# Kernel tuning notes

Hardware: AMD Instinct MI355X
Metric: run time of the kernel (lower is better)

Reference implementation:

```python
import jax, jax.numpy as jnp
import numpy as np

FUSION_RATIO = 0.1


def graph_conv(src, dst, x, W, b, n):
    # DGL GraphConv, norm='both': h = D_in^{-1/2} A D_out^{-1/2} (x W) + b
    ones = jnp.ones((src.shape[0],), x.dtype)
    deg_out = jnp.clip(jax.ops.segment_sum(ones, src, num_segments=n), 1.0)
    deg_in = jnp.clip(jax.ops.segment_sum(ones, dst, num_segments=n), 1.0)
    h = (x @ W) * (deg_out ** -0.5)[:, None]
    agg = jax.ops.segment_sum(h[src], dst, num_segments=n)  # [n, out]
    return agg * (deg_in ** -0.5)[:, None] + b


def norm_embed(e):
    # z-score (unbiased std, matching torch.std) then min-max
    e = (e - e.mean()) / jnp.std(e, ddof=1)
    return (e - e.min()) / (e.max() - e.min())


def setup_inputs() -> dict:
    key = jax.random.key(0)
    ks = jax.random.split(key, 24)
    n_apig, n_fcg = 50000, 100000
    e_apig, e_fcg = 800000, 1600000
    apig_dim, fcg_dim, hidden, united, ncls = 256, 128, 128, 64, 10
    s = 0.05
    inp = {
        'apig_feat': jax.random.normal(ks[0], (n_apig, apig_dim), jnp.float32),
        'fcg_feat': jax.random.normal(ks[1], (n_fcg, fcg_dim), jnp.float32),
        'W_a1': jax.random.normal(ks[2], (apig_dim, hidden), jnp.float32) * s,
        'b_a1': jnp.zeros((hidden,), jnp.float32),
        'W_a2': jax.random.normal(ks[3], (hidden, hidden), jnp.float32) * s,
        'b_a2': jnp.zeros((hidden,), jnp.float32),
        'W_f1': jax.random.normal(ks[4], (fcg_dim, hidden), jnp.float32) * s,
        'b_f1': jnp.zeros((hidden,), jnp.float32),
        'W_f2': jax.random.normal(ks[5], (hidden, hidden), jnp.float32) * s,
        'b_f2': jnp.zeros((hidden,), jnp.float32),
        'W1': jax.random.normal(ks[6], (hidden, united), jnp.float32) * s,
        'b1': jnp.zeros((united,), jnp.float32),
        'W2': jax.random.normal(ks[7], (united, hidden), jnp.float32) * s,
        'b2': jnp.zeros((hidden,), jnp.float32),
        'W_attn': jax.random.normal(ks[8], (hidden, 1), jnp.float32) * s,
        'b_attn': jnp.zeros((1,), jnp.float32),
        'W_cls': jax.random.normal(ks[9], (hidden, ncls), jnp.float32) * s,
        'b_cls': jnp.zeros((ncls,), jnp.float32),
        'apig_src': jax.random.randint(ks[10], (e_apig,), 0, n_apig, jnp.int32),
        'apig_dst': jax.random.randint(ks[11], (e_apig,), 0, n_apig, jnp.int32),
        'fcg_src': jax.random.randint(ks[12], (e_fcg,), 0, n_fcg, jnp.int32),
        'fcg_dst': jax.random.randint(ks[13], (e_fcg,), 0, n_fcg, jnp.int32),
        'n_apig': n_apig,
        'n_fcg': n_fcg,
    }
    return inp


def reference(apig_feat, fcg_feat, W_a1, b_a1, W_a2, b_a2, W_f1, b_f1, W_f2, b_f2,
              W1, b1, W2, b2, W_attn, b_attn, W_cls, b_cls,
              apig_src, apig_dst, fcg_src, fcg_dst, n_apig, n_fcg):
    h_a1 = jax.nn.relu(graph_conv(apig_src, apig_dst, apig_feat, W_a1, b_a1, n_apig))
    h_f1 = jax.nn.relu(graph_conv(fcg_src, fcg_dst, fcg_feat, W_f1, b_f1, n_fcg))
    a_enc = h_a1 @ W1 + b1
    f_enc = h_f1 @ W1 + b1
    a_sum = a_enc.sum(axis=0)
    f_sum = f_enc.sum(axis=0)
    a_enc = a_enc + FUSION_RATIO * f_sum
    f_enc = f_enc + FUSION_RATIO * a_sum
    a_dec = a_enc @ W2 + b2
    f_dec = f_enc @ W2 + b2
    h_a2 = jax.nn.relu(graph_conv(apig_src, apig_dst, a_dec, W_a2, b_a2, n_apig))
    h_f2 = jax.nn.relu(graph_conv(fcg_src, fcg_dst, f_dec, W_f2, b_f2, n_fcg))
    apig_emb = h_a2.mean(axis=0)  # dgl.mean_nodes, single graph -> [hidden]
    fcg_emb = h_f2.max(axis=0)    # dgl.max_nodes -> [hidden]
    a = norm_embed(apig_emb)
    f = norm_embed(fcg_emb)
    wa = jax.nn.softmax(a @ W_attn + b_attn, axis=0)  # [1] -> 1.0
    wf = jax.nn.softmax(f @ W_attn + b_attn, axis=0)
    emb = a * wa + f * wf
    # dropout is identity at inference
    return emb @ W_cls + b_cls
```

## Files before the change

kernel.cpp:

```cpp
#include <hip/hip_runtime.h>
#include <math.h>


typedef __attribute__((ext_vector_type(8))) short bf16x8;
typedef __attribute__((ext_vector_type(8))) unsigned short u16x8;
typedef __attribute__((ext_vector_type(4))) float f32x4;

#define SORT_T 4096

static __device__ inline unsigned short f2bf(float f) {
  unsigned u = __float_as_uint(f);
  unsigned r = (u + 0x7fff + ((u >> 16) & 1)) >> 16;
  return (unsigned short)r;
}
static __device__ inline float bf2f(unsigned short h) {
  return __uint_as_float(((unsigned)h) << 16);
}

static __device__ inline void scan512(int* x) {
  for (int o = 1; o < 512; o <<= 1) {
    int i0 = threadIdx.x, i1 = threadIdx.x + 256;
    int v0 = (i0 >= o) ? x[i0 - o] : 0;
    int v1 = (i1 >= o) ? x[i1 - o] : 0;
    __syncthreads();
    x[i0] += v0;
    x[i1] += v1;
    __syncthreads();
  }
}

__global__ __launch_bounds__(256) void prep_init_kernel(
    const float* __restrict__ W_a1, const float* __restrict__ W_f1,
    const float* __restrict__ W_a2, const float* __restrict__ W_f2,
    const float* __restrict__ W1, const float* __restrict__ W2,
    unsigned short* __restrict__ T_a1, unsigned short* __restrict__ T_f1,
    unsigned short* __restrict__ T_a2, unsigned short* __restrict__ T_f2,
    unsigned short* __restrict__ T1, unsigned short* __restrict__ T2,
    float* __restrict__ s0, float* __restrict__ s1, int ns,
    float* __restrict__ ea, unsigned* __restrict__ ef, int ne,
    int* __restrict__ offs_a, int* __restrict__ offs_src_a, int n_a, int e_a,
    int* __restrict__ offs_f, int* __restrict__ offs_src_f, int n_f, int e_f) {
  if (blockIdx.x == 0 && blockIdx.y == 0) {
    int i = threadIdx.x;
    if (i < ns) { s0[i] = 0.f; s1[i] = 0.f; }
    if (i < ne) { ea[i] = 0.f; ef[i] = 0u; }
    if (i == 0) {
      offs_a[n_a] = e_a;
      offs_src_a[n_a] = e_a;
      offs_f[n_f] = e_f;
      offs_src_f[n_f] = e_f;
    }
  }
  const float* src;
  unsigned short* dst;
  int K, N;
  switch (blockIdx.y) {
    case 0: src = W_a1; dst = T_a1; K = 256; N = 128; break;
    case 1: src = W_f1; dst = T_f1; K = 128; N = 128; break;
    case 2: src = W_a2; dst = T_a2; K = 128; N = 128; break;
    case 3: src = W_f2; dst = T_f2; K = 128; N = 128; break;
    case 4: src = W1;   dst = T1;   K = 128; N = 64;  break;
    default: src = W2;  dst = T2;   K = 64;  N = 128; break;
  }
  int total = K * N;
  for (int idx = blockIdx.x * 256 + threadIdx.x; idx < total; idx += gridDim.x * 256) {
    int n = idx / K, k = idx - n * K;
    dst[idx] = f2bf(src[(size_t)k * N + n]);
  }
}

__global__ __launch_bounds__(256) void hist2_kernel(
    const int* __restrict__ a_dst, const int* __restrict__ f_dst,
    const int* __restrict__ a_src, const int* __restrict__ f_src,
    int e_a, int E, int* __restrict__ blkhistD, int* __restrict__ blkhistS, int B) {
  __shared__ int hD[512], hS[512];
  for (int i = threadIdx.x; i < 512; i += 256) { hD[i] = 0; hS[i] = 0; }
  __syncthreads();
  int base = blockIdx.x * SORT_T;
  int end = base + SORT_T;
  if (end > E) end = E;
  for (int i = base + threadIdx.x; i < end; i += 256) {
    int kD = (i < e_a) ? a_dst[i] : (f_dst[i - e_a] + 65536);
    int kS = (i < e_a) ? a_src[i] : (f_src[i - e_a] + 65536);
    atomicAdd(&hD[kD >> 9], 1);
    atomicAdd(&hS[kS >> 9], 1);
  }
  __syncthreads();
  for (int i = threadIdx.x; i < 512; i += 256) {
    blkhistD[i * B + blockIdx.x] = hD[i];
    blkhistS[i * B + blockIdx.x] = hS[i];
  }
}

__global__ __launch_bounds__(256) void cursor2_kernel(
    int* __restrict__ blkhistD, int* __restrict__ blkhistS, int B,
    int* __restrict__ bintotalD, int* __restrict__ bintotalS) {
  __shared__ int part[256];
  int isD = blockIdx.x < 512;
  int bin = isD ? blockIdx.x : blockIdx.x - 512;
  int* row = (isD ? blkhistD : blkhistS) + (size_t)bin * B;
  int C = (B + 255) / 256;
  int start = threadIdx.x * C;
  int end = start + C;
  if (end > B) end = B;
  int v[8];
  int s = 0;
  for (int j = start; j < end; ++j) {
    v[j - start] = row[j];
    s += v[j - start];
  }
  part[threadIdx.x] = s;
  __syncthreads();
  for (int o = 1; o < 256; o <<= 1) {
    int u = (threadIdx.x >= o) ? part[threadIdx.x - o] : 0;
    __syncthreads();
    part[threadIdx.x] += u;
    __syncthreads();
  }
  int run = part[threadIdx.x] - s;
  for (int j = start; j < end; ++j) {
    row[j] = run;
    run += v[j - start];
  }
  if (threadIdx.x == 255) (isD ? bintotalD : bintotalS)[bin] = part[255];
}

__global__ __launch_bounds__(256) void scatter2_kernel(
    const int* __restrict__ a_dst, const int* __restrict__ f_dst,
    const int* __restrict__ a_src, const int* __restrict__ f_src,
    int e_a, int E, const int* __restrict__ blkhistD, const int* __restrict__ blkhistS,
    int B, const int* __restrict__ bintotalD, const int* __restrict__ bintotalS,
    int* __restrict__ opack, unsigned short* __restrict__ okey) {
  __shared__ int curD[512], curS[512], tmp[512];
  int b = blockIdx.x, tid = threadIdx.x;
  tmp[tid] = bintotalD[tid];
  tmp[tid + 256] = bintotalD[tid + 256];
  __syncthreads();
  scan512(tmp);
  curD[tid] = tmp[tid] - bintotalD[tid] + blkhistD[tid * B + b];
  curD[tid + 256] = tmp[tid + 256] - bintotalD[tid + 256] + blkhistD[(tid + 256) * B + b];
  __syncthreads();
  tmp[tid] = bintotalS[tid];
  tmp[tid + 256] = bintotalS[tid + 256];
  __syncthreads();
  scan512(tmp);
  curS[tid] = tmp[tid] - bintotalS[tid] + blkhistS[tid * B + b];
  curS[tid + 256] = tmp[tid + 256] - bintotalS[tid + 256] + blkhistS[(tid + 256) * B + b];
  __syncthreads();
  int base = b * SORT_T;
  int end = base + SORT_T;
  if (end > E) end = E;
  for (int i = base + tid; i < end; i += 256) {
    int sv = (i < e_a) ? a_src[i] : f_src[i - e_a];
    int kD = (i < e_a) ? a_dst[i] : (f_dst[i - e_a] + 65536);
    int kS = (i < e_a) ? sv : (sv + 65536);
    int posD = atomicAdd(&curD[kD >> 9], 1);
    opack[posD] = ((kD & 511) << 17) | sv;
    int posS = atomicAdd(&curS[kS >> 9], 1);
    okey[posS] = (unsigned short)(kS & 511);
  }
}

__global__ __launch_bounds__(256) void bucket2_kernel(
    const int* __restrict__ kp, const unsigned short* __restrict__ ks,
    const int* __restrict__ bintotalD, const int* __restrict__ bintotalS,
    int E, int e_a,
    int* __restrict__ csr, int* __restrict__ offs_a, int n_a,
    int* __restrict__ offs_f, int n_f,
    int* __restrict__ offs_src_a, int* __restrict__ offs_src_f) {
  __shared__ int sh0[512], sh1[512], sh2[512];
  int tid = threadIdx.x;
  int isD = blockIdx.x < 512;
  int b = isD ? blockIdx.x : blockIdx.x - 512;
  const int* bt = isD ? bintotalD : bintotalS;
  sh0[tid] = bt[tid];
  sh0[tid + 256] = bt[tid + 256];
  __syncthreads();
  scan512(sh0);
  int e = sh0[b];
  int s = e - bt[b];
  sh1[tid] = 0;
  sh1[tid + 256] = 0;
  __syncthreads();
  if (isD) {
    for (int i = s + tid; i < e; i += 256) atomicAdd(&sh1[kp[i] >> 17], 1);
  } else {
    for (int i = s + tid; i < e; i += 256) atomicAdd(&sh1[ks[i]], 1);
  }
  __syncthreads();
  sh2[tid] = sh1[tid];
  sh2[tid + 256] = sh1[tid + 256];
  __syncthreads();
  scan512(sh2);
  for (int low = tid; low < 512; low += 256) {
    int gpos = s + sh2[low] - sh1[low];
    int key = (b << 9) | low;
    if (isD) {
      sh0[low] = gpos;
      if (key < 65536) {
        if (key < n_a) offs_a[key] = gpos;
      } else {
        int v = key - 65536;
        if (v < n_f) offs_f[v] = gpos - e_a;
      }
    } else {
      if (key < 65536) {
        if (key < n_a) offs_src_a[key] = gpos;
      } else {
        int v = key - 65536;
        if (v < n_f) offs_src_f[v] = gpos - e_a;
      }
    }
  }
  if (isD) {
    __syncthreads();
    for (int i = s + tid; i < e; i += 256) {
      int pv = kp[i];
      int pos = atomicAdd(&sh0[pv >> 17], 1);
      csr[pos] = pv & 0x1FFFF;
    }
  }
}

__global__ void isr_kernel(const int* __restrict__ offs_a, const int* __restrict__ offs_src_a,
                           float* __restrict__ io_a, float* __restrict__ ii_a, int n_a,
                           const int* __restrict__ offs_f, const int* __restrict__ offs_src_f,
                           float* __restrict__ io_f, float* __restrict__ ii_f, int n_f) {
  int i = blockIdx.x * blockDim.x + threadIdx.x;
  if (i < n_a) {
    int ci = offs_a[i + 1] - offs_a[i];
    int co = offs_src_a[i + 1] - offs_src_a[i];
    ii_a[i] = 1.0f / sqrtf((float)(ci < 1 ? 1 : ci));
    io_a[i] = 1.0f / sqrtf((float)(co < 1 ? 1 : co));
  }
  if (i < n_f) {
    int ci = offs_f[i + 1] - offs_f[i];
    int co = offs_src_f[i + 1] - offs_src_f[i];
    ii_f[i] = 1.0f / sqrtf((float)(ci < 1 ? 1 : ci));
    io_f[i] = 1.0f / sqrtf((float)(co < 1 ? 1 : co));
  }
}

template <int K, int N, int INBF16, int ADDV>
static __device__ inline void gemm_body(
    const void* __restrict__ A, const unsigned short* __restrict__ Bt,
    unsigned short* __restrict__ C, int M, int bid,
    const float* __restrict__ add_vec, float add_scale,
    const float* __restrict__ rowscale, const float* __restrict__ bias,
    unsigned short* Bs) {
  constexpr int KS = (K < 128) ? K : 128;
  constexpr int KP = KS + 8;
  constexpr int NT = N / 16;
  constexpr int KK = K / 32;
  constexpr int KKS = KS / 32;
  constexpr int NSTAGE = K / KS;
  constexpr int CHUNKS = (N * KS / 8) / 256;

  const int tid = threadIdx.x;
  const int lane = tid & 63, w = tid >> 6;
  const int q = lane >> 4, l16 = lane & 15;
  const int m0 = bid * 64;
  const int m = m0 + w * 16 + l16;
  const int mload = (m < M) ? m : (M - 1);

  bf16x8 af[KK];
  if constexpr (INBF16) {
    const unsigned short* Ar = (const unsigned short*)A + (size_t)mload * K + q * 8;
#pragma unroll
    for (int kk = 0; kk < KK; ++kk)
      af[kk] = *reinterpret_cast<const bf16x8*>(Ar + kk * 32);
  } else {
    const float* Ar = (const float*)A + (size_t)mload * K + q * 8;
    float4 r0[KK], r1[KK];
#pragma unroll
    for (int kk = 0; kk < KK; ++kk) {
      r0[kk] = *reinterpret_cast<const float4*>(Ar + kk * 32);
      r1[kk] = *reinterpret_cast<const float4*>(Ar + kk * 32 + 4);
    }
#pragma unroll
    for (int kk = 0; kk < KK; ++kk) {
      bf16x8 t;
      t[0] = (short)f2bf(r0[kk].x); t[1] = (short)f2bf(r0[kk].y);
      t[2] = (short)f2bf(r0[kk].z); t[3] = (short)f2bf(r0[kk].w);
      t[4] = (short)f2bf(r1[kk].x); t[5] = (short)f2bf(r1[kk].y);
      t[6] = (short)f2bf(r1[kk].z); t[7] = (short)f2bf(r1[kk].w);
      af[kk] = t;
    }
  }
  if constexpr (ADDV) {
#pragma unroll
    for (int kk = 0; kk < KK; ++kk) {
      float4 av0 = *reinterpret_cast<const float4*>(add_vec + kk * 32 + q * 8);
      float4 av1 = *reinterpret_cast<const float4*>(add_vec + kk * 32 + q * 8 + 4);
      u16x8 u = (u16x8)af[kk];
      bf16x8 t;
      t[0] = (short)f2bf(bf2f(u[0]) + add_scale * av0.x);
      t[1] = (short)f2bf(bf2f(u[1]) + add_scale * av0.y);
      t[2] = (short)f2bf(bf2f(u[2]) + add_scale * av0.z);
      t[3] = (short)f2bf(bf2f(u[3]) + add_scale * av0.w);
      t[4] = (short)f2bf(bf2f(u[4]) + add_scale * av1.x);
      t[5] = (short)f2bf(bf2f(u[5]) + add_scale * av1.y);
      t[6] = (short)f2bf(bf2f(u[6]) + add_scale * av1.z);
      t[7] = (short)f2bf(bf2f(u[7]) + add_scale * av1.w);
      af[kk] = t;
    }
  }

  f32x4 acc[NT] = {};
#pragma unroll
  for (int st = 0; st < NSTAGE; ++st) {
    u16x8 breg[CHUNKS];
#pragma unroll
    for (int c = 0; c < CHUNKS; ++c) {
      int idx = c * 256 + tid;
      int n = idx / (KS / 8), kpos = (idx % (KS / 8)) * 8;
      breg[c] = *reinterpret_cast<const u16x8*>(Bt + (size_t)n * K + st * KS + kpos);
    }
    if (st) __syncthreads();
#pragma unroll
    for (int c = 0; c < CHUNKS; ++c) {
      int idx = c * 256 + tid;
      int n = idx / (KS / 8), kpos = (idx % (KS / 8)) * 8;
      *reinterpret_cast<u16x8*>(&Bs[n * KP + kpos]) = breg[c];
    }
    __syncthreads();
#pragma unroll
    for (int kk = 0; kk < KKS; ++kk) {
#pragma unroll
      for (int nt = 0; nt < NT; ++nt) {
        bf16x8 bf =
            *reinterpret_cast<const bf16x8*>(&Bs[(nt * 16 + l16) * KP + kk * 32 + q * 8]);
        acc[nt] =
            __builtin_amdgcn_mfma_f32_16x16x32_bf16(bf, af[st * KKS + kk], acc[nt], 0, 0, 0);
      }
    }
  }

  if (m < M) {
    float rs = rowscale ? rowscale[m] : 1.0f;
#pragma unroll
    for (int nt = 0; nt < NT; ++nt) {
      float4 bv;
      if (bias)
        bv = *reinterpret_cast<const float4*>(bias + nt * 16 + q * 4);
      else
        bv = make_float4(0.f, 0.f, 0.f, 0.f);
      ushort4 st4;
      st4.x = f2bf(fmaf(acc[nt][0], rs, bv.x));
      st4.y = f2bf(fmaf(acc[nt][1], rs, bv.y));
      st4.z = f2bf(fmaf(acc[nt][2], rs, bv.z));
      st4.w = f2bf(fmaf(acc[nt][3], rs, bv.w));
      *reinterpret_cast<ushort4*>(C + (size_t)m * N + nt * 16 + q * 4) = st4;
    }
  }
}

template <int K, int N, int INBF16, int ADDV>
__global__ __launch_bounds__(256) void gemm_bls_kernel(
    const void* __restrict__ A, const unsigned short* __restrict__ Bt,
    unsigned short* __restrict__ C, int M,
    const float* __restrict__ add_vec, float add_scale,
    const float* __restrict__ rowscale, const float* __restrict__ bias) {
  constexpr int KS = (K < 128) ? K : 128;
  __shared__ __align__(16) unsigned short Bs[N * (KS + 8)];
  gemm_body<K, N, INBF16, ADDV>(A, Bt, C, M, blockIdx.x, add_vec, add_scale,
                                rowscale, bias, Bs);
}

template <int K, int N, int INBF16, int ADDV>
__global__ __launch_bounds__(256) void gemm_bls2_kernel(
    const void* __restrict__ A0, const unsigned short* __restrict__ Bt0,
    unsigned short* __restrict__ C0, int M0,
    const void* __restrict__ A1, const unsigned short* __restrict__ Bt1,
    unsigned short* __restrict__ C1, int M1,
    const float* __restrict__ av0, const float* __restrict__ av1, float add_scale,
    const float* __restrict__ rs0, const float* __restrict__ rs1,
    const float* __restrict__ bias, int gblk) {
  constexpr int KS = (K < 128) ? K : 128;
  __shared__ __align__(16) unsigned short Bs[N * (KS + 8)];
  if ((int)blockIdx.x < gblk) {
    gemm_body<K, N, INBF16, ADDV>(A0, Bt0, C0, M0, blockIdx.x, av0, add_scale,
                                  rs0, bias, Bs);
  } else {
    gemm_body<K, N, INBF16, ADDV>(A1, Bt1, C1, M1, blockIdx.x - gblk, av1, add_scale,
                                  rs1, bias, Bs);
  }
}

__global__ __launch_bounds__(256) void agg2_kernel(
    const unsigned short* __restrict__ XW0, const int* __restrict__ offs0,
    const int* __restrict__ csr0, const float* __restrict__ isr0,
    const float* __restrict__ bias0, void* __restrict__ out0, int n0, int mode0,
    const unsigned short* __restrict__ XW1, const int* __restrict__ offs1,
    const int* __restrict__ csr1, const float* __restrict__ isr1,
    const float* __restrict__ bias1, void* __restrict__ out1, int n1, int mode1,
    int nblk0) {
  __shared__ float red[8][128];
  const unsigned short* XW;
  const int *offs, *csr;
  const float *isr_in, *bias;
  void* out;
  int n, mode, bid;
  if ((int)blockIdx.x < nblk0) {
    XW = XW0; offs = offs0; csr = csr0; isr_in = isr0; bias = bias0;
    out = out0; n = n0; mode = mode0; bid = blockIdx.x;
  } else {
    XW = XW1; offs = offs1; csr = csr1; isr_in = isr1; bias = bias1;
    out = out1; n = n1; mode = mode1; bid = blockIdx.x - nblk0;
  }
  int lane = threadIdx.x & 31;
  int g = threadIdx.x >> 5;
  int node = bid * 8 + g;
  float4 o = make_float4(0.f, 0.f, 0.f, 0.f);
  if (node < n) {
    int e0 = offs[node], e1 = offs[node + 1];
    float4 a0 = make_float4(0.f, 0.f, 0.f, 0.f);
    float4 a1 = a0, a2 = a0, a3 = a0;
    int e = e0;
    for (; e + 4 <= e1; e += 4) {
      int s0 = csr[e], s1 = csr[e + 1], s2 = csr[e + 2], s3 = csr[e + 3];
      ushort4 v0 = *reinterpret_cast<const ushort4*>(&XW[(size_t)s0 * 128 + lane * 4]);
      ushort4 v1 = *reinterpret_cast<const ushort4*>(&XW[(size_t)s1 * 128 + lane * 4]);
      ushort4 v2 = *reinterpret_cast<const ushort4*>(&XW[(size_t)s2 * 128 + lane * 4]);
      ushort4 v3 = *reinterpret_cast<const ushort4*>(&XW[(size_t)s3 * 128 + lane * 4]);
      a0.x += bf2f(v0.x); a0.y += bf2f(v0.y); a0.z += bf2f(v0.z); a0.w += bf2f(v0.w);
      a1.x += bf2f(v1.x); a1.y += bf2f(v1.y); a1.z += bf2f(v1.z); a1.w += bf2f(v1.w);
      a2.x += bf2f(v2.x); a2.y += bf2f(v2.y); a2.z += bf2f(v2.z); a2.w += bf2f(v2.w);
      a3.x += bf2f(v3.x); a3.y += bf2f(v3.y); a3.z += bf2f(v3.z); a3.w += bf2f(v3.w);
    }
    for (; e < e1; ++e) {
      int s = csr[e];
      ushort4 v = *reinterpret_cast<const ushort4*>(&XW[(size_t)s * 128 + lane * 4]);
      a0.x += bf2f(v.x); a0.y += bf2f(v.y); a0.z += bf2f(v.z); a0.w += bf2f(v.w);
    }
    float4 acc;
    acc.x = (a0.x + a1.x) + (a2.x + a3.x);
    acc.y = (a0.y + a1.y) + (a2.y + a3.y);
    acc.z = (a0.z + a1.z) + (a2.z + a3.z);
    acc.w = (a0.w + a1.w) + (a2.w + a3.w);
    float sc = isr_in[node];
    float4 b = *reinterpret_cast<const float4*>(&bias[lane * 4]);
    o.x = fmaxf(fmaf(acc.x, sc, b.x), 0.f);
    o.y = fmaxf(fmaf(acc.y, sc, b.y), 0.f);
    o.z = fmaxf(fmaf(acc.z, sc, b.z), 0.f);
    o.w = fmaxf(fmaf(acc.w, sc, b.w), 0.f);
  }
  if (mode == 0) {
    if (node < n) {
      ushort4 st;
      st.x = f2bf(o.x); st.y = f2bf(o.y); st.z = f2bf(o.z); st.w = f2bf(o.w);
      *reinterpret_cast<ushort4*>(&((unsigned short*)out)[(size_t)node * 128 + lane * 4]) = st;
    }
    return;
  }
  red[g][lane * 4 + 0] = o.x;
  red[g][lane * 4 + 1] = o.y;
  red[g][lane * 4 + 2] = o.z;
  red[g][lane * 4 + 3] = o.w;
  __syncthreads();
  if (threadIdx.x < 128) {
    float v = red[0][threadIdx.x];
    if (mode == 1) {
#pragma unroll
      for (int j = 1; j < 8; ++j) v += red[j][threadIdx.x];
    } else {
#pragma unroll
      for (int j = 1; j < 8; ++j) v = fmaxf(v, red[j][threadIdx.x]);
    }
    ((float*)out)[(size_t)bid * 128 + threadIdx.x] = v;
  }
}

__global__ __launch_bounds__(256) void colsum2_kernel(
    const unsigned short* __restrict__ X0, float* __restrict__ out0, int n0,
    const unsigned short* __restrict__ X1, float* __restrict__ out1, int n1,
    int ncol) {
  __shared__ float s[256];
  const unsigned short* X;
  float* out;
  int n, bid;
  if ((int)blockIdx.x < 256) { X = X0; out = out0; n = n0; bid = blockIdx.x; }
  else { X = X1; out = out1; n = n1; bid = blockIdx.x - 256; }
  int col = threadIdx.x % ncol;
  int rpb = 256 / ncol;
  int rb = threadIdx.x / ncol;
  float acc = 0.f;
  for (int r = bid * rpb + rb; r < n; r += 256 * rpb)
    acc += bf2f(X[(size_t)r * ncol + col]);
  s[threadIdx.x] = acc;
  __syncthreads();
  if (threadIdx.x < ncol) {
    float v = 0.f;
    for (int i = 0; i < rpb; ++i) v += s[threadIdx.x + i * ncol];
    atomicAdd(&out[col], v);
  }
}

__global__ __launch_bounds__(256) void colfin_kernel(
    const float* __restrict__ Pa, float* __restrict__ emb_a, int na,
    const float* __restrict__ Pf, unsigned* __restrict__ emb_f, int nf, int ncol) {
  __shared__ float s[256];
  int isSum = blockIdx.x < 256;
  const float* X = isSum ? Pa : Pf;
  int n = isSum ? na : nf;
  int bid = isSum ? blockIdx.x : blockIdx.x - 256;
  int col = threadIdx.x % ncol;
  int rpb = 256 / ncol;
  int rb = threadIdx.x / ncol;
  float acc = 0.f;
  if (isSum) {
    for (int r = bid * rpb + rb; r < n; r += 256 * rpb) acc += X[(size_t)r * ncol + col];
  } else {
    for (int r = bid * rpb + rb; r < n; r += 256 * rpb)
      acc = fmaxf(acc, X[(size_t)r * ncol + col]);
  }
  s[threadIdx.x] = acc;
  __syncthreads();
  if (threadIdx.x < ncol) {
    if (isSum) {
      float v = 0.f;
      for (int i = 0; i < rpb; ++i) v += s[threadIdx.x + i * ncol];
      atomicAdd(&emb_a[col], v);
    } else {
      float v = s[threadIdx.x];
      for (int i = 1; i < rpb; ++i) v = fmaxf(v, s[threadIdx.x + i * ncol]);
      atomicMax(&emb_f[col], __float_as_uint(v));
    }
  }
}

__global__ __launch_bounds__(128) void final_kernel(
    const float* __restrict__ emb_a_sum, const unsigned* __restrict__ emb_f_bits,
    const float* __restrict__ W_cls, const float* __restrict__ b_cls,
    float* __restrict__ out, float inv_n_apig, int ncls) {
  __shared__ float red[128];
  __shared__ float emb[128];
  int t = threadIdx.x;
  float a = emb_a_sum[t] * inv_n_apig;
  float f = __uint_as_float(emb_f_bits[t]);

  float vals[2] = {a, f};
  float norms[2];
#pragma unroll
  for (int which = 0; which < 2; ++which) {
    float x = vals[which];
    red[t] = x;
    __syncthreads();
    for (int o = 64; o > 0; o >>= 1) {
      if (t < o) red[t] += red[t + o];
      __syncthreads();
    }
    float mean = red[0] / 128.f;
    __syncthreads();
    float d = x - mean;
    red[t] = d * d;
    __syncthreads();
    for (int o = 64; o > 0; o >>= 1) {
      if (t < o) red[t] += red[t + o];
      __syncthreads();
    }
    float stdv = sqrtf(red[0] / 127.f);
    __syncthreads();
    float z = d / stdv;
    red[t] = z;
    __syncthreads();
    for (int o = 64; o > 0; o >>= 1) {
      if (t < o) red[t] = fminf(red[t], red[t + o]);
      __syncthreads();
    }
    float zmin = red[0];
    __syncthreads();
    red[t] = z;
    __syncthreads();
    for (int o = 64; o > 0; o >>= 1) {
      if (t < o) red[t] = fmaxf(red[t], red[t + o]);
      __syncthreads();
    }
    float zmax = red[0];
    __syncthreads();
    norms[which] = (z - zmin) / (zmax - zmin);
  }

  emb[t] = norms[0] + norms[1];
  __syncthreads();
  if (t < ncls) {
    float acc = b_cls[t];
    for (int k = 0; k < 128; ++k) acc = fmaf(emb[k], W_cls[k * ncls + t], acc);
    out[t] = acc;
  }
}

extern "C" void kernel_launch(void* const* d_in, const int* in_sizes, int n_in,
                              void* d_out, int out_size, void* d_ws, size_t ws_size,
                              hipStream_t stream) {
  const float* apig_feat = (const float*)d_in[0];
  const float* fcg_feat = (const float*)d_in[1];
  const float* W_a1 = (const float*)d_in[2];
  const float* b_a1 = (const float*)d_in[3];
  const float* W_a2 = (const float*)d_in[4];
  const float* b_a2 = (const float*)d_in[5];
  const float* W_f1 = (const float*)d_in[6];
  const float* b_f1 = (const float*)d_in[7];
  const float* W_f2 = (const float*)d_in[8];
  const float* b_f2 = (const float*)d_in[9];
  const float* W1 = (const float*)d_in[10];
  const float* b1 = (const float*)d_in[11];
  const float* W2 = (const float*)d_in[12];
  const float* b2 = (const float*)d_in[13];
  const float* W_cls = (const float*)d_in[16];
  const float* b_cls = (const float*)d_in[17];
  const int* a_src = (const int*)d_in[18];
  const int* a_dst = (const int*)d_in[19];
  const int* f_src = (const int*)d_in[20];
  const int* f_dst = (const int*)d_in[21];

  const int hidden = in_sizes[3];
  const int united = in_sizes[11];
  const int ncls = in_sizes[17];
  const int apig_dim = in_sizes[2] / hidden;
  const int fcg_dim = in_sizes[6] / hidden;
  const int n_a = in_sizes[0] / apig_dim;
  const int n_f = in_sizes[1] / fcg_dim;
  const int e_a = in_sizes[18];
  const int e_f = in_sizes[20];

  char* w = (char*)d_ws;
  auto alloc = [&](size_t bytes) -> void* {
    void* p = (void*)w;
    w += (bytes + 255) & ~(size_t)255;
    return p;
  };
  const int E_tot = e_a + e_f;
  const int B = (E_tot + SORT_T - 1) / SORT_T;
  const int nblkA = (n_a + 7) / 8, nblkF = (n_f + 7) / 8;

  float* isr_out_a = (float*)alloc((size_t)n_a * 4);
  float* isr_in_a = (float*)alloc((size_t)n_a * 4);
  float* isr_out_f = (float*)alloc((size_t)n_f * 4);
  float* isr_in_f = (float*)alloc((size_t)n_f * 4);
  int* offs_a = (int*)alloc((size_t)(n_a + 1) * 4);
  int* offs_f = (int*)alloc((size_t)(n_f + 1) * 4);
  int* offs_src_a = (int*)alloc((size_t)(n_a + 1) * 4);
  int* offs_src_f = (int*)alloc((size_t)(n_f + 1) * 4);
  int* kp = (int*)alloc((size_t)E_tot * 4);
  unsigned short* okey = (unsigned short*)alloc((size_t)E_tot * 2);
  int* csr = (int*)alloc((size_t)E_tot * 4);
  int* blkhistD = (int*)alloc((size_t)512 * B * 4);
  int* blkhistS = (int*)alloc((size_t)512 * B * 4);
  int* bintotalD = (int*)alloc((size_t)512 * 4);
  int* bintotalS = (int*)alloc((size_t)512 * 4);
  unsigned short* G_a = (unsigned short*)alloc((size_t)n_a * hidden * 2);
  unsigned short* H_a = (unsigned short*)alloc((size_t)n_a * hidden * 2);
  unsigned short* G_f = (unsigned short*)alloc((size_t)n_f * hidden * 2);
  unsigned short* H_f = (unsigned short*)alloc((size_t)n_f * hidden * 2);
  float* P_a = (float*)alloc((size_t)nblkA * hidden * 4);
  float* P_f = (float*)alloc((size_t)nblkF * hidden * 4);
  unsigned short* E_a = G_a;
  unsigned short* E_f = G_f;
  float* a_sum = (float*)alloc((size_t)united * 4);
  float* f_sum = (float*)alloc((size_t)united * 4);
  float* emb_a = (float*)alloc((size_t)hidden * 4);
  unsigned* emb_f = (unsigned*)alloc((size_t)hidden * 4);
  unsigned short* T_a1 = (unsigned short*)alloc((size_t)apig_dim * hidden * 2);
  unsigned short* T_f1 = (unsigned short*)alloc((size_t)fcg_dim * hidden * 2);
  unsigned short* T_a2 = (unsigned short*)alloc((size_t)hidden * hidden * 2);
  unsigned short* T_f2 = (unsigned short*)alloc((size_t)hidden * hidden * 2);
  unsigned short* T1 = (unsigned short*)alloc((size_t)hidden * united * 2);
  unsigned short* T2 = (unsigned short*)alloc((size_t)united * hidden * 2);
  int* csr_a = csr;
  int* csr_f = csr + e_a;
  (void)ws_size;
  (void)n_in;
  (void)out_size;

  dim3 blk(256);

  prep_init_kernel<<<dim3(32, 6), blk, 0, stream>>>(
      W_a1, W_f1, W_a2, W_f2, W1, W2, T_a1, T_f1, T_a2, T_f2, T1, T2,
      a_sum, f_sum, united, emb_a, emb_f, hidden,
      offs_a, offs_src_a, n_a, e_a, offs_f, offs_src_f, n_f, e_f);

  hist2_kernel<<<B, blk, 0, stream>>>(a_dst, f_dst, a_src, f_src, e_a, E_tot,
                                      blkhistD, blkhistS, B);
  cursor2_kernel<<<1024, blk, 0, stream>>>(blkhistD, blkhistS, B, bintotalD, bintotalS);
  scatter2_kernel<<<B, blk, 0, stream>>>(a_dst, f_dst, a_src, f_src, e_a, E_tot,
                                         blkhistD, blkhistS, B, bintotalD, bintotalS,
                                         kp, okey);
  bucket2_kernel<<<1024, blk, 0, stream>>>(kp, okey, bintotalD, bintotalS, E_tot, e_a,
                                           csr, offs_a, n_a, offs_f, n_f,
                                           offs_src_a, offs_src_f);
  isr_kernel<<<(n_f + 255) / 256, blk, 0, stream>>>(offs_a, offs_src_a, isr_out_a, isr_in_a,
                                                    n_a, offs_f, offs_src_f, isr_out_f,
                                                    isr_in_f, n_f);

  const int ga = (n_a + 63) / 64, gf = (n_f + 63) / 64;

  gemm_bls_kernel<256, 128, 0, 0><<<ga, blk, 0, stream>>>(
      apig_feat, T_a1, G_a, n_a, nullptr, 0.f, isr_out_a, nullptr);
  gemm_bls_kernel<128, 128, 0, 0><<<gf, blk, 0, stream>>>(
      fcg_feat, T_f1, G_f, n_f, nullptr, 0.f, isr_out_f, nullptr);
  agg2_kernel<<<nblkA + nblkF, blk, 0, stream>>>(
      G_a, offs_a, csr_a, isr_in_a, b_a1, H_a, n_a, 0,
      G_f, offs_f, csr_f, isr_in_f, b_f1, H_f, n_f, 0, nblkA);
  gemm_bls2_kernel<128, 64, 1, 0><<<ga + gf, blk, 0, stream>>>(
      H_a, T1, E_a, n_a, H_f, T1, E_f, n_f,
      nullptr, nullptr, 0.f, nullptr, nullptr, b1, ga);
  colsum2_kernel<<<512, blk, 0, stream>>>(E_a, a_sum, n_a, E_f, f_sum, n_f, united);
  gemm_bls2_kernel<64, 128, 1, 1><<<ga + gf, blk, 0, stream>>>(
      E_a, T2, H_a, n_a, E_f, T2, H_f, n_f,
      f_sum, a_sum, 0.1f, nullptr, nullptr, b2, ga);
  gemm_bls2_kernel<128, 128, 1, 0><<<ga + gf, blk, 0, stream>>>(
      H_a, T_a2, G_a, n_a, H_f, T_f2, G_f, n_f,
      nullptr, nullptr, 0.f, isr_out_a, isr_out_f, nullptr, ga);
  agg2_kernel<<<nblkA + nblkF, blk, 0, stream>>>(
      G_a, offs_a, csr_a, isr_in_a, b_a2, P_a, n_a, 1,
      G_f, offs_f, csr_f, isr_in_f, b_f2, P_f, n_f, 2, nblkA);
  colfin_kernel<<<512, blk, 0, stream>>>(P_a, emb_a, nblkA, P_f, emb_f, nblkF, hidden);
  final_kernel<<<1, 128, 0, stream>>>(emb_a, emb_f, W_cls, b_cls, (float*)d_out,
                                      1.0f / (float)n_a, ncls);
}
```

Baseline: 570.7 us.

## Merge small kernels to cut launches: fuse hist/prep, degree norms, conv1 GEMMs, final

Folds weight transpose/init into the histogram kernel, computes inverse-sqrt degrees directly in the bucket kernel (dropping the src-offset arrays and the isr kernel), merges the two first-layer GEMMs into one launch, and fuses the final classifier into the column-reduction kernel using a last-block-done counter. The aim is to remove several kernel launches and their serialization gaps, plus some offset-array traffic. The last-block pattern adds an atomic counter and threadfence, and correctness relies on counter reset every call.

After: 585.9 us. 2.7% more time.

```diff
diff --git a/kernel.cpp b/kernel.cpp
--- a/kernel.cpp
+++ b/kernel.cpp
@@ -29,7 +29,124 @@
   }
 }
 
-__global__ __launch_bounds__(256) void prep_init_kernel(
+template <int K, int N, int INBF16, int ADDV>
+static __device__ inline void gemm_body(
+    const void* __restrict__ A, const unsigned short* __restrict__ Bt,
+    unsigned short* __restrict__ C, int M, int bid,
+    const float* __restrict__ add_vec, float add_scale,
+    const float* __restrict__ rowscale, const float* __restrict__ bias,
+    unsigned short* Bs) {
+  constexpr int KS = (K < 128) ? K : 128;
+  constexpr int KP = KS + 8;
+  constexpr int NT = N / 16;
+  constexpr int KK = K / 32;
+  constexpr int KKS = KS / 32;
+  constexpr int NSTAGE = K / KS;
+  constexpr int CHUNKS = (N * KS / 8) / 256;
+
+  const int tid = threadIdx.x;
+  const int lane = tid & 63, w = tid >> 6;
+  const int q = lane >> 4, l16 = lane & 15;
+  const int m0 = bid * 64;
+  const int m = m0 + w * 16 + l16;
+  const int mload = (m < M) ? m : (M - 1);
+
+  bf16x8 af[KK];
+  if constexpr (INBF16) {
+    const unsigned short* Ar = (const unsigned short*)A + (size_t)mload * K + q * 8;
+#pragma unroll
+    for (int kk = 0; kk < KK; ++kk)
+      af[kk] = *reinterpret_cast<const bf16x8*>(Ar + kk * 32);
+  } else {
+    const float* Ar = (const float*)A + (size_t)mload * K + q * 8;
+    float4 r0[KK], r1[KK];
+#pragma unroll
+    for (int kk = 0; kk < KK; ++kk) {
+      r0[kk] = *reinterpret_cast<const float4*>(Ar + kk * 32);
+      r1[kk] = *reinterpret_cast<const float4*>(Ar + kk * 32 + 4);
+    }
+#pragma unroll
+    for (int kk = 0; kk < KK; ++kk) {
+      bf16x8 t;
+      t[0] = (short)f2bf(r0[kk].x); t[1] = (short)f2bf(r0[kk].y);
+      t[2] = (short)f2bf(r0[kk].z); t[3] = (short)f2bf(r0[kk].w);
+      t[4] = (short)f2bf(r1[kk].x); t[5] = (short)f2bf(r1[kk].y);
+      t[6] = (short)f2bf(r1[kk].z); t[7] = (short)f2bf(r1[kk].w);
+      af[kk] = t;
+    }
+  }
+  if constexpr (ADDV) {
+#pragma unroll
+    for (int kk = 0; kk < KK; ++kk) {
+      float4 av0 = *reinterpret_cast<const float4*>(add_vec + kk * 32 + q * 8);
+      float4 av1 = *reinterpret_cast<const float4*>(add_vec + kk * 32 + q * 8 + 4);
+      u16x8 u = (u16x8)af[kk];
+      bf16x8 t;
+      t[0] = (short)f2bf(bf2f(u[0]) + add_scale * av0.x);
+      t[1] = (short)f2bf(bf2f(u[1]) + add_scale * av0.y);
+      t[2] = (short)f2bf(bf2f(u[2]) + add_scale * av0.z);
+      t[3] = (short)f2bf(bf2f(u[3]) + add_scale * av0.w);
+      t[4] = (short)f2bf(bf2f(u[4]) + add_scale * av1.x);
+      t[5] = (short)f2bf(bf2f(u[5]) + add_scale * av1.y);
+      t[6] = (short)f2bf(bf2f(u[6]) + add_scale * av1.z);
+      t[7] = (short)f2bf(bf2f(u[7]) + add_scale * av1.w);
+      af[kk] = t;
+    }
+  }
+
+  f32x4 acc[NT] = {};
+#pragma unroll
+  for (int st = 0; st < NSTAGE; ++st) {
+    u16x8 breg[CHUNKS];
+#pragma unroll
+    for (int c = 0; c < CHUNKS; ++c) {
+      int idx = c * 256 + tid;
+      int n = idx / (KS / 8), kpos = (idx % (KS / 8)) * 8;
+      breg[c] = *reinterpret_cast<const u16x8*>(Bt + (size_t)n * K + st * KS + kpos);
+    }
+    if (st) __syncthreads();
+#pragma unroll
+    for (int c = 0; c < CHUNKS; ++c) {
+      int idx = c * 256 + tid;
+      int n = idx / (KS / 8), kpos = (idx % (KS / 8)) * 8;
+      *reinterpret_cast<u16x8*>(&Bs[n * KP + kpos]) = breg[c];
+    }
+    __syncthreads();
+#pragma unroll
+    for (int kk = 0; kk < KKS; ++kk) {
+#pragma unroll
+      for (int nt = 0; nt < NT; ++nt) {
+        bf16x8 bf =
+            *reinterpret_cast<const bf16x8*>(&Bs[(nt * 16 + l16) * KP + kk * 32 + q * 8]);
+        acc[nt] =
+            __builtin_amdgcn_mfma_f32_16x16x32_bf16(bf, af[st * KKS + kk], acc[nt], 0, 0, 0);
+      }
+    }
+  }
+
+  if (m < M) {
+    float rs = rowscale ? rowscale[m] : 1.0f;
+#pragma unroll
+    for (int nt = 0; nt < NT; ++nt) {
+      float4 bv;
+      if (bias)
+        bv = *reinterpret_cast<const float4*>(bias + nt * 16 + q * 4);
+      else
+        bv = make_float4(0.f, 0.f, 0.f, 0.f);
+      ushort4 st4;
+      st4.x = f2bf(fmaf(acc[nt][0], rs, bv.x));
+      st4.y = f2bf(fmaf(acc[nt][1], rs, bv.y));
+      st4.z = f2bf(fmaf(acc[nt][2], rs, bv.z));
+      st4.w = f2bf(fmaf(acc[nt][3], rs, bv.w));
+      *reinterpret_cast<ushort4*>(C + (size_t)m * N + nt * 16 + q * 4) = st4;
+    }
+  }
+}
+
+__global__ __launch_bounds__(256) void histprep_kernel(
+    const int* __restrict__ a_dst, const int* __restrict__ f_dst,
+    const int* __restrict__ a_src, const int* __restrict__ f_src,
+    int e_a, int E, int* __restrict__ blkhistD, int* __restrict__ blkhistS, int B,
     const float* __restrict__ W_a1, const float* __restrict__ W_f1,
     const float* __restrict__ W_a2, const float* __restrict__ W_f2,
     const float* __restrict__ W1, const float* __restrict__ W2,
@@ -38,23 +155,44 @@
     unsigned short* __restrict__ T1, unsigned short* __restrict__ T2,
     float* __restrict__ s0, float* __restrict__ s1, int ns,
     float* __restrict__ ea, unsigned* __restrict__ ef, int ne,
-    int* __restrict__ offs_a, int* __restrict__ offs_src_a, int n_a, int e_a,
-    int* __restrict__ offs_f, int* __restrict__ offs_src_f, int n_f, int e_f) {
-  if (blockIdx.x == 0 && blockIdx.y == 0) {
+    int* __restrict__ offs_a, int n_a, int* __restrict__ offs_f, int n_f,
+    int e_f_rel, int* __restrict__ done_cnt) {
+  __shared__ int hD[512], hS[512];
+  if ((int)blockIdx.x < B) {
+    for (int i = threadIdx.x; i < 512; i += 256) { hD[i] = 0; hS[i] = 0; }
+    __syncthreads();
+    int base = blockIdx.x * SORT_T;
+    int end = base + SORT_T;
+    if (end > E) end = E;
+    for (int i = base + threadIdx.x; i < end; i += 256) {
+      int kD = (i < e_a) ? a_dst[i] : (f_dst[i - e_a] + 65536);
+      int kS = (i < e_a) ? a_src[i] : (f_src[i - e_a] + 65536);
+      atomicAdd(&hD[kD >> 9], 1);
+      atomicAdd(&hS[kS >> 9], 1);
+    }
+    __syncthreads();
+    for (int i = threadIdx.x; i < 512; i += 256) {
+      blkhistD[i * B + blockIdx.x] = hD[i];
+      blkhistS[i * B + blockIdx.x] = hS[i];
+    }
+    return;
+  }
+  int pb = blockIdx.x - B;
+  if (pb == 0) {
     int i = threadIdx.x;
     if (i < ns) { s0[i] = 0.f; s1[i] = 0.f; }
     if (i < ne) { ea[i] = 0.f; ef[i] = 0u; }
     if (i == 0) {
       offs_a[n_a] = e_a;
-      offs_src_a[n_a] = e_a;
-      offs_f[n_f] = e_f;
-      offs_src_f[n_f] = e_f;
-    }
-  }
+      offs_f[n_f] = e_f_rel;
+      *done_cnt = 0;
+    }
+  }
+  int py = pb >> 5, px = pb & 31;
   const float* src;
   unsigned short* dst;
   int K, N;
-  switch (blockIdx.y) {
+  switch (py) {
     case 0: src = W_a1; dst = T_a1; K = 256; N = 128; break;
     case 1: src = W_f1; dst = T_f1; K = 128; N = 128; break;
     case 2: src = W_a2; dst = T_a2; K = 128; N = 128; break;
@@ -63,32 +201,9 @@
     default: src = W2;  dst = T2;   K = 64;  N = 128; break;
   }
   int total = K * N;
-  for (int idx = blockIdx.x * 256 + threadIdx.x; idx < total; idx += gridDim.x * 256) {
+  for (int idx = px * 256 + threadIdx.x; idx < total; idx += 32 * 256) {
     int n = idx / K, k = idx - n * K;
     dst[idx] = f2bf(src[(size_t)k * N + n]);
-  }
-}
-
-__global__ __launch_bounds__(256) void hist2_kernel(
-    const int* __restrict__ a_dst, const int* __restrict__ f_dst,
-    const int* __restrict__ a_src, const int* __restrict__ f_src,
-    int e_a, int E, int* __restrict__ blkhistD, int* __restrict__ blkhistS, int B) {
-  __shared__ int hD[512], hS[512];
-  for (int i = threadIdx.x; i < 512; i += 256) { hD[i] = 0; hS[i] = 0; }
-  __syncthreads();
-  int base = blockIdx.x * SORT_T;
-  int end = base + SORT_T;
-  if (end > E) end = E;
-  for (int i = base + threadIdx.x; i < end; i += 256) {
-    int kD = (i < e_a) ? a_dst[i] : (f_dst[i - e_a] + 65536);
-    int kS = (i < e_a) ? a_src[i] : (f_src[i - e_a] + 65536);
-    atomicAdd(&hD[kD >> 9], 1);
-    atomicAdd(&hS[kS >> 9], 1);
-  }
-  __syncthreads();
-  for (int i = threadIdx.x; i < 512; i += 256) {
-    blkhistD[i * B + blockIdx.x] = hD[i];
-    blkhistS[i * B + blockIdx.x] = hS[i];
   }
 }
 
@@ -167,7 +282,8 @@
     int E, int e_a,
     int* __restrict__ csr, int* __restrict__ offs_a, int n_a,
     int* __restrict__ offs_f, int n_f,
-    int* __restrict__ offs_src_a, int* __restrict__ offs_src_f) {
+    float* __restrict__ ii_a, float* __restrict__ ii_f,
+    float* __restrict__ io_a, float* __restrict__ io_f) {
   __shared__ int sh0[512], sh1[512], sh2[512];
   int tid = threadIdx.x;
   int isD = blockIdx.x < 512;
@@ -193,22 +309,24 @@
   __syncthreads();
   scan512(sh2);
   for (int low = tid; low < 512; low += 256) {
-    int gpos = s + sh2[low] - sh1[low];
+    int c = sh1[low];
+    int gpos = s + sh2[low] - c;
     int key = (b << 9) | low;
+    float inv = 1.0f / sqrtf((float)(c < 1 ? 1 : c));
     if (isD) {
       sh0[low] = gpos;
       if (key < 65536) {
-        if (key < n_a) offs_a[key] = gpos;
+        if (key < n_a) { offs_a[key] = gpos; ii_a[key] = inv; }
       } else {
         int v = key - 65536;
-        if (v < n_f) offs_f[v] = gpos - e_a;
+        if (v < n_f) { offs_f[v] = gpos - e_a; ii_f[v] = inv; }
       }
     } else {
       if (key < 65536) {
-        if (key < n_a) offs_src_a[key] = gpos;
+        if (key < n_a) io_a[key] = inv;
       } else {
         int v = key - 65536;
-        if (v < n_f) offs_src_f[v] = gpos - e_a;
+        if (v < n_f) io_f[v] = inv;
       }
     }
   }
@@ -222,149 +340,20 @@
   }
 }
 
-__global__ void isr_kernel(const int* __restrict__ offs_a, const int* __restrict__ offs_src_a,
-                           float* __restrict__ io_a, float* __restrict__ ii_a, int n_a,
-                           const int* __restrict__ offs_f, const int* __restrict__ offs_src_f,
-                           float* __restrict__ io_f, float* __restrict__ ii_f, int n_f) {
-  int i = blockIdx.x * blockDim.x + threadIdx.x;
-  if (i < n_a) {
-    int ci = offs_a[i + 1] - offs_a[i];
-    int co = offs_src_a[i + 1] - offs_src_a[i];
-    ii_a[i] = 1.0f / sqrtf((float)(ci < 1 ? 1 : ci));
-    io_a[i] = 1.0f / sqrtf((float)(co < 1 ? 1 : co));
-  }
-  if (i < n_f) {
-    int ci = offs_f[i + 1] - offs_f[i];
-    int co = offs_src_f[i + 1] - offs_src_f[i];
-    ii_f[i] = 1.0f / sqrtf((float)(ci < 1 ? 1 : ci));
-    io_f[i] = 1.0f / sqrtf((float)(co < 1 ? 1 : co));
-  }
-}
-
-template <int K, int N, int INBF16, int ADDV>
-static __device__ inline void gemm_body(
-    const void* __restrict__ A, const unsigned short* __restrict__ Bt,
-    unsigned short* __restrict__ C, int M, int bid,
-    const float* __restrict__ add_vec, float add_scale,
-    const float* __restrict__ rowscale, const float* __restrict__ bias,
-    unsigned short* Bs) {
-  constexpr int KS = (K < 128) ? K : 128;
-  constexpr int KP = KS + 8;
-  constexpr int NT = N / 16;
-  constexpr int KK = K / 32;
-  constexpr int KKS = KS / 32;
-  constexpr int NSTAGE = K / KS;
-  constexpr int CHUNKS = (N * KS / 8) / 256;
-
-  const int tid = threadIdx.x;
-  const int lane = tid & 63, w = tid >> 6;
-  const int q = lane >> 4, l16 = lane & 15;
-  const int m0 = bid * 64;
-  const int m = m0 + w * 16 + l16;
-  const int mload = (m < M) ? m : (M - 1);
-
-  bf16x8 af[KK];
-  if constexpr (INBF16) {
-    const unsigned short* Ar = (const unsigned short*)A + (size_t)mload * K + q * 8;
-#pragma unroll
-    for (int kk = 0; kk < KK; ++kk)
-      af[kk] = *reinterpret_cast<const bf16x8*>(Ar + kk * 32);
+__global__ __launch_bounds__(256) void gemm_conv1_kernel(
+    const float* __restrict__ A0, const unsigned short* __restrict__ Bt0,
+    unsigned short* __restrict__ C0, int M0, const float* __restrict__ rs0,
+    const float* __restrict__ A1, const unsigned short* __restrict__ Bt1,
+    unsigned short* __restrict__ C1, int M1, const float* __restrict__ rs1,
+    int gblk) {
+  __shared__ __align__(16) unsigned short Bs[128 * 136];
+  if ((int)blockIdx.x < gblk) {
+    gemm_body<256, 128, 0, 0>(A0, Bt0, C0, M0, blockIdx.x, nullptr, 0.f, rs0,
+                              nullptr, Bs);
   } else {
-    const float* Ar = (const float*)A + (size_t)mload * K + q * 8;
-    float4 r0[KK], r1[KK];
-#pragma unroll
-    for (int kk = 0; kk < KK; ++kk) {
-      r0[kk] = *reinterpret_cast<const float4*>(Ar + kk * 32);
-      r1[kk] = *reinterpret_cast<const float4*>(Ar + kk * 32 + 4);
-    }
-#pragma unroll
-    for (int kk = 0; kk < KK; ++kk) {
-      bf16x8 t;
-      t[0] = (short)f2bf(r0[kk].x); t[1] = (short)f2bf(r0[kk].y);
-      t[2] = (short)f2bf(r0[kk].z); t[3] = (short)f2bf(r0[kk].w);
-      t[4] = (short)f2bf(r1[kk].x); t[5] = (short)f2bf(r1[kk].y);
-      t[6] = (short)f2bf(r1[kk].z); t[7] = (short)f2bf(r1[kk].w);
-      af[kk] = t;
-    }
-  }
-  if constexpr (ADDV) {
-#pragma unroll
-    for (int kk = 0; kk < KK; ++kk) {
-      float4 av0 = *reinterpret_cast<const float4*>(add_vec + kk * 32 + q * 8);
-      float4 av1 = *reinterpret_cast<const float4*>(add_vec + kk * 32 + q * 8 + 4);
-      u16x8 u = (u16x8)af[kk];
-      bf16x8 t;
-      t[0] = (short)f2bf(bf2f(u[0]) + add_scale * av0.x);
-      t[1] = (short)f2bf(bf2f(u[1]) + add_scale * av0.y);
-      t[2] = (short)f2bf(bf2f(u[2]) + add_scale * av0.z);
-      t[3] = (short)f2bf(bf2f(u[3]) + add_scale * av0.w);
-      t[4] = (short)f2bf(bf2f(u[4]) + add_scale * av1.x);
-      t[5] = (short)f2bf(bf2f(u[5]) + add_scale * av1.y);
-      t[6] = (short)f2bf(bf2f(u[6]) + add_scale * av1.z);
-      t[7] = (short)f2bf(bf2f(u[7]) + add_scale * av1.w);
-      af[kk] = t;
-    }
-  }
-
-  f32x4 acc[NT] = {};
-#pragma unroll
-  for (int st = 0; st < NSTAGE; ++st) {
-    u16x8 breg[CHUNKS];
-#pragma unroll
-    for (int c = 0; c < CHUNKS; ++c) {
-      int idx = c * 256 + tid;
-      int n = idx / (KS / 8), kpos = (idx % (KS / 8)) * 8;
-      breg[c] = *reinterpret_cast<const u16x8*>(Bt + (size_t)n * K + st * KS + kpos);
-    }
-    if (st) __syncthreads();
-#pragma unroll
-    for (int c = 0; c < CHUNKS; ++c) {
-      int idx = c * 256 + tid;
-      int n = idx / (KS / 8), kpos = (idx % (KS / 8)) * 8;
-      *reinterpret_cast<u16x8*>(&Bs[n * KP + kpos]) = breg[c];
-    }
-    __syncthreads();
-#pragma unroll
-    for (int kk = 0; kk < KKS; ++kk) {
-#pragma unroll
-      for (int nt = 0; nt < NT; ++nt) {
-        bf16x8 bf =
-            *reinterpret_cast<const bf16x8*>(&Bs[(nt * 16 + l16) * KP + kk * 32 + q * 8]);
-        acc[nt] =
-            __builtin_amdgcn_mfma_f32_16x16x32_bf16(bf, af[st * KKS + kk], acc[nt], 0, 0, 0);
-      }
-    }
-  }
-
-  if (m < M) {
-    float rs = rowscale ? rowscale[m] : 1.0f;
-#pragma unroll
-    for (int nt = 0; nt < NT; ++nt) {
-      float4 bv;
-      if (bias)
-        bv = *reinterpret_cast<const float4*>(bias + nt * 16 + q * 4);
-      else
-        bv = make_float4(0.f, 0.f, 0.f, 0.f);
-      ushort4 st4;
-      st4.x = f2bf(fmaf(acc[nt][0], rs, bv.x));
-      st4.y = f2bf(fmaf(acc[nt][1], rs, bv.y));
-      st4.z = f2bf(fmaf(acc[nt][2], rs, bv.z));
-      st4.w = f2bf(fmaf(acc[nt][3], rs, bv.w));
-      *reinterpret_cast<ushort4*>(C + (size_t)m * N + nt * 16 + q * 4) = st4;
-    }
-  }
-}
-
-template <int K, int N, int INBF16, int ADDV>
-__global__ __launch_bounds__(256) void gemm_bls_kernel(
-    const void* __restrict__ A, const unsigned short* __restrict__ Bt,
-    unsigned short* __restrict__ C, int M,
-    const float* __restrict__ add_vec, float add_scale,
-    const float* __restrict__ rowscale, const float* __restrict__ bias) {
-  constexpr int KS = (K < 128) ? K : 128;
-  __shared__ __align__(16) unsigned short Bs[N * (KS + 8)];
-  gemm_body<K, N, INBF16, ADDV>(A, Bt, C, M, blockIdx.x, add_vec, add_scale,
-                                rowscale, bias, Bs);
+    gemm_body<128, 128, 0, 0>(A1, Bt1, C1, M1, blockIdx.x - gblk, nullptr, 0.f, rs1,
+                              nullptr, Bs);
+  }
 }
 
 template <int K, int N, int INBF16, int ADDV>
@@ -496,73 +485,83 @@
   }
 }
 
-__global__ __launch_bounds__(256) void colfin_kernel(
+__global__ __launch_bounds__(256) void colfin_final_kernel(
     const float* __restrict__ Pa, float* __restrict__ emb_a, int na,
-    const float* __restrict__ Pf, unsigned* __restrict__ emb_f, int nf, int ncol) {
+    const float* __restrict__ Pf, unsigned* __restrict__ emb_f, int nf, int ncol,
+    int* __restrict__ done_cnt, const float* __restrict__ W_cls,
+    const float* __restrict__ b_cls, float* __restrict__ out,
+    float inv_n_apig, int ncls) {
   __shared__ float s[256];
-  int isSum = blockIdx.x < 256;
-  const float* X = isSum ? Pa : Pf;
-  int n = isSum ? na : nf;
-  int bid = isSum ? blockIdx.x : blockIdx.x - 256;
-  int col = threadIdx.x % ncol;
-  int rpb = 256 / ncol;
-  int rb = threadIdx.x / ncol;
-  float acc = 0.f;
-  if (isSum) {
-    for (int r = bid * rpb + rb; r < n; r += 256 * rpb) acc += X[(size_t)r * ncol + col];
-  } else {
-    for (int r = bid * rpb + rb; r < n; r += 256 * rpb)
-      acc = fmaxf(acc, X[(size_t)r * ncol + col]);
-  }
-  s[threadIdx.x] = acc;
-  __syncthreads();
-  if (threadIdx.x < ncol) {
+  {
+    int isSum = blockIdx.x < 256;
+    const float* X = isSum ? Pa : Pf;
+    int n = isSum ? na : nf;
+    int bid = isSum ? blockIdx.x : blockIdx.x - 256;
+    int col = threadIdx.x % ncol;
+    int rpb = 256 / ncol;
+    int rb = threadIdx.x / ncol;
+    float acc = 0.f;
     if (isSum) {
-      float v = 0.f;
-      for (int i = 0; i < rpb; ++i) v += s[threadIdx.x + i * ncol];
-      atomicAdd(&emb_a[col], v);
+      for (int r = bid * rpb + rb; r < n; r += 256 * rpb) acc += X[(size_t)r * ncol + col];
     } else {
-      float v = s[threadIdx.x];
-      for (int i = 1; i < rpb; ++i) v = fmaxf(v, s[threadIdx.x + i * ncol]);
-      atomicMax(&emb_f[col], __float_as_uint(v));
-    }
-  }
-}
-
-__global__ __launch_bounds__(128) void final_kernel(
-    const float* __restrict__ emb_a_sum, const unsigned* __restrict__ emb_f_bits,
-    const float* __restrict__ W_cls, const float* __restrict__ b_cls,
-    float* __restrict__ out, float inv_n_apig, int ncls) {
+      for (int r = bid * rpb + rb; r < n; r += 256 * rpb)
+        acc = fmaxf(acc, X[(size_t)r * ncol + col]);
+    }
+    s[threadIdx.x] = acc;
+    __syncthreads();
+    if (threadIdx.x < ncol) {
+      if (isSum) {
+        float v = 0.f;
+        for (int i = 0; i < rpb; ++i) v += s[threadIdx.x + i * ncol];
+        atomicAdd(&emb_a[col], v);
+      } else {
+        float v = s[threadIdx.x];
+        for (int i = 1; i < rpb; ++i) v = fmaxf(v, s[threadIdx.x + i * ncol]);
+        atomicMax(&emb_f[col], __float_as_uint(v));
+      }
+    }
+  }
+  __threadfence();
+  __shared__ int lastv;
+  if (threadIdx.x == 0) lastv = (atomicAdd(done_cnt, 1) == 511) ? 1 : 0;
+  __syncthreads();
+  if (!lastv) return;
+
   __shared__ float red[128];
-  __shared__ float emb[128];
+  __shared__ float embs[128];
   int t = threadIdx.x;
-  float a = emb_a_sum[t] * inv_n_apig;
-  float f = __uint_as_float(emb_f_bits[t]);
-
+  float a = 0.f, f = 0.f;
+  if (t < 128) {
+    a = __hip_atomic_load(&emb_a[t], __ATOMIC_RELAXED, __HIP_MEMORY_SCOPE_AGENT) *
+        inv_n_apig;
+    unsigned fb = __hip_atomic_load(&emb_f[t], __ATOMIC_RELAXED, __HIP_MEMORY_SCOPE_AGENT);
+    f = __uint_as_float(fb);
+  }
   float vals[2] = {a, f};
-  float norms[2];
+  float norms[2] = {0.f, 0.f};
 #pragma unroll
   for (int which = 0; which < 2; ++which) {
     float x = vals[which];
-    red[t] = x;
+    __syncthreads();
+    if (t < 128) red[t] = x;
     __syncthreads();
     for (int o = 64; o > 0; o >>= 1) {
       if (t < o) red[t] += red[t + o];
       __syncthreads();
     }
     float mean = red[0] / 128.f;
-    __syncthreads();
     float d = x - mean;
-    red[t] = d * d;
+    __syncthreads();
+    if (t < 128) red[t] = d * d;
     __syncthreads();
     for (int o = 64; o > 0; o >>= 1) {
       if (t < o) red[t] += red[t + o];
       __syncthreads();
     }
     float stdv = sqrtf(red[0] / 127.f);
-    __syncthreads();
     float z = d / stdv;
-    red[t] = z;
+    __syncthreads();
+    if (t < 128) red[t] = z;
     __syncthreads();
     for (int o = 64; o > 0; o >>= 1) {
       if (t < o) red[t] = fminf(red[t], red[t + o]);
@@ -570,22 +569,21 @@
     }
     float zmin = red[0];
     __syncthreads();
-    red[t] = z;
+    if (t < 128) red[t] = z;
     __syncthreads();
     for (int o = 64; o > 0; o >>= 1) {
       if (t < o) red[t] = fmaxf(red[t], red[t + o]);
       __syncthreads();
     }
     float zmax = red[0];
-    __syncthreads();
     norms[which] = (z - zmin) / (zmax - zmin);
   }
-
-  emb[t] = norms[0] + norms[1];
+  __syncthreads();
+  if (t < 128) embs[t] = norms[0] + norms[1];
   __syncthreads();
   if (t < ncls) {
     float acc = b_cls[t];
-    for (int k = 0; k < 128; ++k) acc = fmaf(emb[k], W_cls[k * ncls + t], acc);
+    for (int k = 0; k < 128; ++k) acc = fmaf(embs[k], W_cls[k * ncls + t], acc);
     out[t] = acc;
   }
 }
@@ -640,8 +638,6 @@
   float* isr_in_f = (float*)alloc((size_t)n_f * 4);
   int* offs_a = (int*)alloc((size_t)(n_a + 1) * 4);
   int* offs_f = (int*)alloc((size_t)(n_f + 1) * 4);
-  int* offs_src_a = (int*)alloc((size_t)(n_a + 1) * 4);
-  int* offs_src_f = (int*)alloc((size_t)(n_f + 1) * 4);
   int* kp = (int*)alloc((size_t)E_tot * 4);
   unsigned short* okey = (unsigned short*)alloc((size_t)E_tot * 2);
   int* csr = (int*)alloc((size_t)E_tot * 4);
@@ -661,6 +657,7 @@
   float* f_sum = (float*)alloc((size_t)united * 4);
   float* emb_a = (float*)alloc((size_t)hidden * 4);
   unsigned* emb_f = (unsigned*)alloc((size_t)hidden * 4);
+  int* done_cnt = (int*)alloc(256);
   unsigned short* T_a1 = (unsigned short*)alloc((size_t)apig_dim * hidden * 2);
   unsigned short* T_f1 = (unsigned short*)alloc((size_t)fcg_dim * hidden * 2);
   unsigned short* T_a2 = (unsigned short*)alloc((size_t)hidden * hidden * 2);
@@ -674,31 +671,23 @@
   (void)out_size;
 
   dim3 blk(256);
-
-  prep_init_kernel<<<dim3(32, 6), blk, 0, stream>>>(
+  const int ga = (n_a + 63) / 64, gf = (n_f + 63) / 64;
+
+  histprep_kernel<<<B + 192, blk, 0, stream>>>(
+      a_dst, f_dst, a_src, f_src, e_a, E_tot, blkhistD, blkhistS, B,
       W_a1, W_f1, W_a2, W_f2, W1, W2, T_a1, T_f1, T_a2, T_f2, T1, T2,
       a_sum, f_sum, united, emb_a, emb_f, hidden,
-      offs_a, offs_src_a, n_a, e_a, offs_f, offs_src_f, n_f, e_f);
-
-  hist2_kernel<<<B, blk, 0, stream>>>(a_dst, f_dst, a_src, f_src, e_a, E_tot,
-                                      blkhistD, blkhistS, B);
+      offs_a, n_a, offs_f, n_f, e_f, done_cnt);
   cursor2_kernel<<<1024, blk, 0, stream>>>(blkhistD, blkhistS, B, bintotalD, bintotalS);
   scatter2_kernel<<<B, blk, 0, stream>>>(a_dst, f_dst, a_src, f_src, e_a, E_tot,
                                          blkhistD, blkhistS, B, bintotalD, bintotalS,
                                          kp, okey);
   bucket2_kernel<<<1024, blk, 0, stream>>>(kp, okey, bintotalD, bintotalS, E_tot, e_a,
                                            csr, offs_a, n_a, offs_f, n_f,
-                                           offs_src_a, offs_src_f);
-  isr_kernel<<<(n_f + 255) / 256, blk, 0, stream>>>(offs_a, offs_src_a, isr_out_a, isr_in_a,
-                                                    n_a, offs_f, offs_src_f, isr_out_f,
-                                                    isr_in_f, n_f);
-
-  const int ga = (n_a + 63) / 64, gf = (n_f + 63) / 64;
-
-  gemm_bls_kernel<256, 128, 0, 0><<<ga, blk, 0, stream>>>(
-      apig_feat, T_a1, G_a, n_a, nullptr, 0.f, isr_out_a, nullptr);
-  gemm_bls_kernel<128, 128, 0, 0><<<gf, blk, 0, stream>>>(
-      fcg_feat, T_f1, G_f, n_f, nullptr, 0.f, isr_out_f, nullptr);
+                                           isr_in_a, isr_in_f, isr_out_a, isr_out_f);
+  gemm_conv1_kernel<<<ga + gf, blk, 0, stream>>>(
+      apig_feat, T_a1, G_a, n_a, isr_out_a,
+      fcg_feat, T_f1, G_f, n_f, isr_out_f, ga);
   agg2_kernel<<<nblkA + nblkF, blk, 0, stream>>>(
       G_a, offs_a, csr_a, isr_in_a, b_a1, H_a, n_a, 0,
       G_f, offs_f, csr_f, isr_in_f, b_f1, H_f, n_f, 0, nblkA);
@@ -715,7 +704,7 @@
   agg2_kernel<<<nblkA + nblkF, blk, 0, stream>>>(
       G_a, offs_a, csr_a, isr_in_a, b_a2, P_a, n_a, 1,
       G_f, offs_f, csr_f, isr_in_f, b_f2, P_f, n_f, 2, nblkA);
-  colfin_kernel<<<512, blk, 0, stream>>>(P_a, emb_a, nblkA, P_f, emb_f, nblkF, hidden);
-  final_kernel<<<1, 128, 0, stream>>>(emb_a, emb_f, W_cls, b_cls, (float*)d_out,
-                                      1.0f / (float)n_a, ncls);
-}
+  colfin_final_kernel<<<512, blk, 0, stream>>>(
+      P_a, emb_a, nblkA, P_f, emb_f, nblkF, hidden,
+      done_cnt, W_cls, b_cls, (float*)d_out, 1.0f / (float)n_a, ncls);
+}
```
